# Kernel tuning notes

Measured on AMD Instinct MI355X. Metric: run time of the kernel, lower is better.

Reference implementation:

```python
import jax, jax.numpy as jnp
import numpy as np

B = 64          # number of graph pairs
NODES_PER = 128 # nodes per graph (both sides)
DIM = 256

def setup_inputs() -> dict:
    key = jax.random.key(0)
    k1, k2 = jax.random.split(key)
    N = B * NODES_PER
    left_graph_emb = jax.random.normal(k1, (N, DIM), dtype=jnp.float32)
    right_graph_emb = jax.random.normal(k2, (N, DIM), dtype=jnp.float32)
    # contiguous sorted segment ids, every graph non-empty (matches torch cumsum slicing)
    left_x_batch = jnp.repeat(jnp.arange(B, dtype=jnp.int64), NODES_PER)
    right_x_batch = jnp.repeat(jnp.arange(B, dtype=jnp.int64), NODES_PER)
    return {"left_graph_emb": left_graph_emb, "right_graph_emb": right_graph_emb,
            "left_x_batch": left_x_batch, "right_x_batch": right_x_batch}

def _match(left_emb, right_emb, left_b, right_b):
    # pair mask: node i (left) attends node j (right) only within the same graph
    mask = left_b[:, None] == right_b[None, :]            # [Nl, Nr]
    scores = left_emb @ right_emb.T                        # [Nl, Nr]
    neg = jnp.asarray(-1e30, scores.dtype)
    masked = jnp.where(mask, scores, neg)
    # row softmax (dim=1 in torch) -> right-attended emb per left node
    right_atten = jax.nn.softmax(masked, axis=1) @ right_emb      # [Nl, D]
    # col softmax (dim=0 in torch) -> left-attended emb per right node
    left_atten = jax.nn.softmax(masked, axis=0).T @ left_emb      # [Nr, D]
    # sigmoid gates from inner products
    wl = jax.nn.sigmoid(jnp.sum(left_emb * right_atten, axis=1, keepdims=True))
    wr = jax.nn.sigmoid(jnp.sum(right_emb * left_atten, axis=1, keepdims=True))
    return wl * left_emb, wr * right_emb

def reference(left_graph_emb, right_graph_emb, left_x_batch, right_x_batch):
    ml, mr = _match(left_graph_emb, right_graph_emb, left_x_batch, right_x_batch)
    left_global = jax.ops.segment_sum(ml, left_x_batch, num_segments=B)    # [B, D]
    right_global = jax.ops.segment_sum(mr, right_x_batch, num_segments=B)  # [B, D]
    return left_global, right_global
```

## Files before the change

### kernel.cpp

```cpp
#include <hip/hip_runtime.h>
#include <hip/hip_bf16.h>

#define NGRAPH 64
#define NPER   128
#define DIM    256

typedef __attribute__((ext_vector_type(8))) short bf16x8;
typedef __attribute__((ext_vector_type(4))) float f32x4;

__device__ __forceinline__ float bf2f(short s) {
    union { unsigned u; float f; } v; v.u = ((unsigned)(unsigned short)s) << 16;
    return v.f;
}

__device__ __forceinline__ bf16x8 cvt8(const float4 a, const float4 b) {
    __hip_bfloat162 p0 = __float22bfloat162_rn({a.x, a.y});
    __hip_bfloat162 p1 = __float22bfloat162_rn({a.z, a.w});
    __hip_bfloat162 p2 = __float22bfloat162_rn({b.x, b.y});
    __hip_bfloat162 p3 = __float22bfloat162_rn({b.z, b.w});
    union { __hip_bfloat162 h[4]; bf16x8 v; } u;
    u.h[0] = p0; u.h[1] = p1; u.h[2] = p2; u.h[3] = p3;
    return u.v;
}

__global__ __launch_bounds__(512, 1)
void match_gate_kernel(const float* __restrict__ left,
                       const float* __restrict__ right,
                       float* __restrict__ out) {
    __shared__ __align__(16) short Ls[NPER * DIM];
    __shared__ __align__(16) short Rs[NPER * DIM];
    __shared__ float wq[NPER];
    __shared__ float red[4][128];

    const int j    = blockIdx.x;
    const int g    = (((j >> 5) & 7) << 3) | (j & 7);
    const int sub  = (j >> 3) & 3;
    const int side = sub >> 1;
    const int dh   = sub & 1;

    const float* Lg = left  + (size_t)g * NPER * DIM;
    const float* Rg = right + (size_t)g * NPER * DIM;

    const int tid = threadIdx.x;

    #pragma unroll
    for (int b = 0; b < 4; ++b) {
        const float* src_panel = (b < 2) ? Lg : Rg;
        short* dst_panel = (b < 2) ? Ls : Rs;
        float4 f[8];
        int row[4], k8[4];
        #pragma unroll
        for (int u = 0; u < 4; ++u) {
            const int cc = (b & 1) * 2048 + u * 512 + tid;
            row[u] = cc >> 5;
            k8[u]  = cc & 31;
            const float* s = src_panel + row[u] * DIM + k8[u] * 8;
            f[2 * u]     = *(const float4*)(s);
            f[2 * u + 1] = *(const float4*)(s + 4);
        }
        #pragma unroll
        for (int u = 0; u < 4; ++u) {
            const bf16x8 h = cvt8(f[2 * u], f[2 * u + 1]);
            const int byte = row[u] * (DIM * 2) + ((k8[u] * 16) ^ ((row[u] & 7) << 4));
            *(bf16x8*)((char*)dst_panel + byte) = h;
        }
    }
    __syncthreads();

    const short* Qs = side ? Rs : Ls;
    const short* Ks = side ? Ls : Rs;

    const int wave = tid >> 6;
    const int lane = tid & 63;
    const int row0 = wave * 16;
    const int lr   = lane & 15;
    const int lkb  = (lane >> 4) * 16;

    f32x4 acc[8];
    #pragma unroll
    for (int c = 0; c < 8; ++c) acc[c] = (f32x4){0.f, 0.f, 0.f, 0.f};

    const int arow = row0 + lr;
    const char* aBase = (const char*)Qs + arow * (DIM * 2);
    const int aswz = (arow & 7) << 4;

    #pragma unroll
    for (int ks = 0; ks < 8; ++ks) {
        const bf16x8 a = *(const bf16x8*)(aBase + ((ks * 64 + lkb) ^ aswz));
        #pragma unroll
        for (int c = 0; c < 8; ++c) {
            const int brow = c * 16 + lr;
            const bf16x8 bb = *(const bf16x8*)((const char*)Ks + brow * (DIM * 2)
                                               + ((ks * 64 + lkb) ^ ((brow & 7) << 4)));
            acc[c] = __builtin_amdgcn_mfma_f32_16x16x32_bf16(a, bb, acc[c], 0, 0, 0);
        }
    }

    #pragma unroll
    for (int r = 0; r < 4; ++r) {
        float m = acc[0][r];
        #pragma unroll
        for (int c = 1; c < 8; ++c) m = fmaxf(m, acc[c][r]);
        #pragma unroll
        for (int off = 1; off < 16; off <<= 1) m = fmaxf(m, __shfl_xor(m, off, 64));
        float se = 0.f, wsum = 0.f;
        #pragma unroll
        for (int c = 0; c < 8; ++c) {
            const float e = __expf(acc[c][r] - m);
            se += e; wsum += e * acc[c][r];
        }
        #pragma unroll
        for (int off = 1; off < 16; off <<= 1) {
            se   += __shfl_xor(se, off, 64);
            wsum += __shfl_xor(wsum, off, 64);
        }
        if ((lane & 15) == 0)
            wq[row0 + (lane >> 4) * 4 + r] = 1.f / (1.f + __expf(-(wsum / se)));
    }
    __syncthreads();

    const int dd   = tid & 127;
    const int part = tid >> 7;
    const int dgl  = dh * 128 + dd;
    float sum = 0.f;
    #pragma unroll 8
    for (int i = part * 32; i < part * 32 + 32; ++i) {
        const short s = *(const short*)((const char*)Qs + i * (DIM * 2)
                                        + ((2 * dgl) ^ ((i & 7) << 4)));
        sum += wq[i] * bf2f(s);
    }
    red[part][dd] = sum;
    __syncthreads();
    if (tid < 128) {
        float* outp = out + (size_t)side * (NGRAPH * DIM) + (size_t)g * DIM + dh * 128;
        outp[tid] = red[0][tid] + red[1][tid] + red[2][tid] + red[3][tid];
    }
}

extern "C" void kernel_launch(void* const* d_in, const int* in_sizes, int n_in,
                              void* d_out, int out_size, void* d_ws, size_t ws_size,
                              hipStream_t stream) {
    const float* left  = (const float*)d_in[0];
    const float* right = (const float*)d_in[1];
    float* out = (float*)d_out;
    match_gate_kernel<<<256, 512, 0, stream>>>(left, right, out);
}
```

Measured before the change: 13.21 us.

## Compute row and column softmax gates from one shared score tile per block

Each block now computes the L·R^T score tile once and derives both the row-softmax gates (left side) and the column-softmax gates (right side), merging partial softmax statistics (max, sum, weighted sum) across waves with an online-softmax combine. Blocks grow to 1024 threads split into row tiles and column halves. Each block still recomputes the full GEMM for its graph but writes a 64-wide output quarter for both sides. Before, separate blocks handled the left and right sides, and each one recomputed the GEMM. The change removes that duplicate GEMM work and halves per-thread MFMA accumulators, at the cost of extra shared-memory partial buffers, merge arithmetic and column shuffles.

```diff
diff --git a/kernel.cpp b/kernel.cpp
--- a/kernel.cpp
+++ b/kernel.cpp
@@ -23,20 +23,29 @@
     return u.v;
 }
 
-__global__ __launch_bounds__(512, 1)
-void match_gate_kernel(const float* __restrict__ left,
+__device__ __forceinline__ void sm_merge(float& m, float& se, float& ws,
+                                         float mo, float seo, float wso) {
+    const float M = fmaxf(m, mo);
+    const float a = __expf(m - M), b = __expf(mo - M);
+    se = a * se + b * seo;
+    ws = a * ws + b * wso;
+    m = M;
+}
+
+__global__ __launch_bounds__(1024, 1)
+void match_both_kernel(const float* __restrict__ left,
                        const float* __restrict__ right,
                        float* __restrict__ out) {
     __shared__ __align__(16) short Ls[NPER * DIM];
     __shared__ __align__(16) short Rs[NPER * DIM];
-    __shared__ float wq[NPER];
-    __shared__ float red[4][128];
+    __shared__ float rowpart[2][NPER][3];
+    __shared__ float colpart[8][NPER][3];
+    __shared__ float gl[NPER], gr[NPER];
+    __shared__ float red[2][8][64];
 
-    const int j    = blockIdx.x;
-    const int g    = (((j >> 5) & 7) << 3) | (j & 7);
-    const int sub  = (j >> 3) & 3;
-    const int side = sub >> 1;
-    const int dh   = sub & 1;
+    const int j  = blockIdx.x;
+    const int g  = (((j >> 5) & 7) << 3) | (j & 7);
+    const int dq = (j >> 3) & 3;
 
     const float* Lg = left  + (size_t)g * NPER * DIM;
     const float* Rg = right + (size_t)g * NPER * DIM;
@@ -44,14 +53,14 @@
     const int tid = threadIdx.x;
 
     #pragma unroll
-    for (int b = 0; b < 4; ++b) {
-        const float* src_panel = (b < 2) ? Lg : Rg;
-        short* dst_panel = (b < 2) ? Ls : Rs;
+    for (int b = 0; b < 2; ++b) {
+        const float* src_panel = b ? Rg : Lg;
+        short* dst_panel = b ? Rs : Ls;
         float4 f[8];
         int row[4], k8[4];
         #pragma unroll
         for (int u = 0; u < 4; ++u) {
-            const int cc = (b & 1) * 2048 + u * 512 + tid;
+            const int cc = u * 1024 + tid;
             row[u] = cc >> 5;
             k8[u]  = cc & 31;
             const float* s = src_panel + row[u] * DIM + k8[u] * 8;
@@ -67,45 +76,43 @@
     }
     __syncthreads();
 
-    const short* Qs = side ? Rs : Ls;
-    const short* Ks = side ? Ls : Rs;
-
     const int wave = tid >> 6;
     const int lane = tid & 63;
-    const int row0 = wave * 16;
+    const int t    = wave & 7;
+    const int ch   = wave >> 3;
+    const int row0 = t * 16;
     const int lr   = lane & 15;
     const int lkb  = (lane >> 4) * 16;
 
-    f32x4 acc[8];
+    f32x4 acc[4];
     #pragma unroll
-    for (int c = 0; c < 8; ++c) acc[c] = (f32x4){0.f, 0.f, 0.f, 0.f};
+    for (int c = 0; c < 4; ++c) acc[c] = (f32x4){0.f, 0.f, 0.f, 0.f};
 
     const int arow = row0 + lr;
-    const char* aBase = (const char*)Qs + arow * (DIM * 2);
+    const char* aBase = (const char*)Ls + arow * (DIM * 2);
     const int aswz = (arow & 7) << 4;
 
     #pragma unroll
     for (int ks = 0; ks < 8; ++ks) {
         const bf16x8 a = *(const bf16x8*)(aBase + ((ks * 64 + lkb) ^ aswz));
         #pragma unroll
-        for (int c = 0; c < 8; ++c) {
-            const int brow = c * 16 + lr;
-            const bf16x8 bb = *(const bf16x8*)((const char*)Ks + brow * (DIM * 2)
+        for (int c = 0; c < 4; ++c) {
+            const int brow = ch * 64 + c * 16 + lr;
+            const bf16x8 bb = *(const bf16x8*)((const char*)Rs + brow * (DIM * 2)
                                                + ((ks * 64 + lkb) ^ ((brow & 7) << 4)));
             acc[c] = __builtin_amdgcn_mfma_f32_16x16x32_bf16(a, bb, acc[c], 0, 0, 0);
         }
     }
 
+
     #pragma unroll
     for (int r = 0; r < 4; ++r) {
-        float m = acc[0][r];
-        #pragma unroll
-        for (int c = 1; c < 8; ++c) m = fmaxf(m, acc[c][r]);
+        float m = fmaxf(fmaxf(acc[0][r], acc[1][r]), fmaxf(acc[2][r], acc[3][r]));
         #pragma unroll
         for (int off = 1; off < 16; off <<= 1) m = fmaxf(m, __shfl_xor(m, off, 64));
         float se = 0.f, wsum = 0.f;
         #pragma unroll
-        for (int c = 0; c < 8; ++c) {
+        for (int c = 0; c < 4; ++c) {
             const float e = __expf(acc[c][r] - m);
             se += e; wsum += e * acc[c][r];
         }
@@ -114,26 +121,70 @@
             se   += __shfl_xor(se, off, 64);
             wsum += __shfl_xor(wsum, off, 64);
         }
-        if ((lane & 15) == 0)
-            wq[row0 + (lane >> 4) * 4 + r] = 1.f / (1.f + __expf(-(wsum / se)));
+        if ((lane & 15) == 0) {
+            const int rr = row0 + (lane >> 4) * 4 + r;
+            rowpart[ch][rr][0] = m; rowpart[ch][rr][1] = se; rowpart[ch][rr][2] = wsum;
+        }
+    }
+
+    #pragma unroll
+    for (int c = 0; c < 4; ++c) {
+        float m = fmaxf(fmaxf(acc[c][0], acc[c][1]), fmaxf(acc[c][2], acc[c][3]));
+        float se = 0.f, wsum = 0.f;
+        #pragma unroll
+        for (int r = 0; r < 4; ++r) {
+            const float e = __expf(acc[c][r] - m);
+            se += e; wsum += e * acc[c][r];
+        }
+        #pragma unroll
+        for (int off = 16; off < 64; off <<= 1) {
+            const float mo  = __shfl_xor(m, off, 64);
+            const float seo = __shfl_xor(se, off, 64);
+            const float wso = __shfl_xor(wsum, off, 64);
+            sm_merge(m, se, wsum, mo, seo, wso);
+        }
+        if (lane < 16) {
+            const int jj = ch * 64 + c * 16 + lr;
+            colpart[t][jj][0] = m; colpart[t][jj][1] = se; colpart[t][jj][2] = wsum;
+        }
     }
     __syncthreads();
 
-    const int dd   = tid & 127;
-    const int part = tid >> 7;
-    const int dgl  = dh * 128 + dd;
+    if (tid < NPER) {
+        float m = rowpart[0][tid][0], se = rowpart[0][tid][1], wsum = rowpart[0][tid][2];
+        sm_merge(m, se, wsum, rowpart[1][tid][0], rowpart[1][tid][1], rowpart[1][tid][2]);
+        gl[tid] = 1.f / (1.f + __expf(-(wsum / se)));
+    } else if (tid < 2 * NPER) {
+        const int jj = tid - NPER;
+        float m = colpart[0][jj][0], se = colpart[0][jj][1], wsum = colpart[0][jj][2];
+        #pragma unroll
+        for (int s = 1; s < 8; ++s)
+            sm_merge(m, se, wsum, colpart[s][jj][0], colpart[s][jj][1], colpart[s][jj][2]);
+        gr[jj] = 1.f / (1.f + __expf(-(wsum / se)));
+    }
+    __syncthreads();
+
+    const int side = tid >> 9;
+    const int d    = tid & 63;
+    const int part = (tid >> 6) & 7;
+    const short* P  = side ? Rs : Ls;
+    const float* gg = side ? gr : gl;
+    const int dgl = dq * 64 + d;
     float sum = 0.f;
-    #pragma unroll 8
-    for (int i = part * 32; i < part * 32 + 32; ++i) {
-        const short s = *(const short*)((const char*)Qs + i * (DIM * 2)
+    #pragma unroll
+    for (int i = part * 16; i < part * 16 + 16; ++i) {
+        const short s = *(const short*)((const char*)P + i * (DIM * 2)
                                         + ((2 * dgl) ^ ((i & 7) << 4)));
-        sum += wq[i] * bf2f(s);
+        sum += gg[i] * bf2f(s);
     }
-    red[part][dd] = sum;
+    red[side][part][d] = sum;
     __syncthreads();
     if (tid < 128) {
-        float* outp = out + (size_t)side * (NGRAPH * DIM) + (size_t)g * DIM + dh * 128;
-        outp[tid] = red[0][tid] + red[1][tid] + red[2][tid] + red[3][tid];
+        const int sd = tid >> 6, dd = tid & 63;
+        float s = 0.f;
+        #pragma unroll
+        for (int p = 0; p < 8; ++p) s += red[sd][p][dd];
+        out[(size_t)sd * (NGRAPH * DIM) + (size_t)g * DIM + dq * 64 + dd] = s;
     }
 }
 
@@ -143,5 +194,5 @@
     const float* left  = (const float*)d_in[0];
     const float* right = (const float*)d_in[1];
     float* out = (float*)d_out;
-    match_gate_kernel<<<256, 512, 0, stream>>>(left, right, out);
+    match_both_kernel<<<256, 1024, 0, stream>>>(left, right, out);
 }
```

New measurement: 16.32 us. 23.5% more time.

## Split K-dimension staging to overlap second-half loads with first-half MFMAs

Applied to the files above, without the earlier changes.

The global-to-LDS staging of the L and R panels is split along the feature dimension. The first half of K (columns 0-127) is loaded and converted first, followed by a barrier. The second half is then loaded into registers while the MFMAs for k-steps 0-3 run on the first half, then stored, and after a second barrier the remaining k-steps complete. This hides part of the global load latency behind compute, at the cost of an extra barrier and higher register pressure from holding loads in flight during MFMAs.

```diff
diff --git a/kernel.cpp b/kernel.cpp
--- a/kernel.cpp
+++ b/kernel.cpp
@@ -44,25 +44,24 @@
     const int tid = threadIdx.x;
 
     #pragma unroll
-    for (int b = 0; b < 4; ++b) {
-        const float* src_panel = (b < 2) ? Lg : Rg;
-        short* dst_panel = (b < 2) ? Ls : Rs;
+    for (int b = 0; b < 2; ++b) {
         float4 f[8];
         int row[4], k8[4];
         #pragma unroll
         for (int u = 0; u < 4; ++u) {
-            const int cc = (b & 1) * 2048 + u * 512 + tid;
-            row[u] = cc >> 5;
-            k8[u]  = cc & 31;
-            const float* s = src_panel + row[u] * DIM + k8[u] * 8;
+            const int cc = (b * 4 + u) * 512 + tid;
+            row[u] = (cc >> 4) & 127;
+            k8[u]  = cc & 15;
+            const float* s = (b ? Rg : Lg) + row[u] * DIM + k8[u] * 8;
             f[2 * u]     = *(const float4*)(s);
             f[2 * u + 1] = *(const float4*)(s + 4);
         }
+        short* dst = b ? Rs : Ls;
         #pragma unroll
         for (int u = 0; u < 4; ++u) {
             const bf16x8 h = cvt8(f[2 * u], f[2 * u + 1]);
             const int byte = row[u] * (DIM * 2) + ((k8[u] * 16) ^ ((row[u] & 7) << 4));
-            *(bf16x8*)((char*)dst_panel + byte) = h;
+            *(bf16x8*)((char*)dst + byte) = h;
         }
     }
     __syncthreads();
@@ -84,8 +83,7 @@
     const char* aBase = (const char*)Qs + arow * (DIM * 2);
     const int aswz = (arow & 7) << 4;
 
-    #pragma unroll
-    for (int ks = 0; ks < 8; ++ks) {
+    auto do_mfma = [&](int ks) {
         const bf16x8 a = *(const bf16x8*)(aBase + ((ks * 64 + lkb) ^ aswz));
         #pragma unroll
         for (int c = 0; c < 8; ++c) {
@@ -94,7 +92,49 @@
                                                + ((ks * 64 + lkb) ^ ((brow & 7) << 4)));
             acc[c] = __builtin_amdgcn_mfma_f32_16x16x32_bf16(a, bb, acc[c], 0, 0, 0);
         }
+    };
+
+    {
+        float4 fA[8];
+        int rA[4], kA[4];
+        #pragma unroll
+        for (int u = 0; u < 4; ++u) {
+            const int cc = u * 512 + tid;
+            rA[u] = (cc >> 4) & 127;
+            kA[u] = 16 + (cc & 15);
+            const float* s = Lg + rA[u] * DIM + kA[u] * 8;
+            fA[2 * u]     = *(const float4*)(s);
+            fA[2 * u + 1] = *(const float4*)(s + 4);
+        }
+        do_mfma(0); do_mfma(1);
+        #pragma unroll
+        for (int u = 0; u < 4; ++u) {
+            const bf16x8 h = cvt8(fA[2 * u], fA[2 * u + 1]);
+            const int byte = rA[u] * (DIM * 2) + ((kA[u] * 16) ^ ((rA[u] & 7) << 4));
+            *(bf16x8*)((char*)Ls + byte) = h;
+        }
+        float4 fB[8];
+        int rB[4], kB[4];
+        #pragma unroll
+        for (int u = 0; u < 4; ++u) {
+            const int cc = (4 + u) * 512 + tid;
+            rB[u] = (cc >> 4) & 127;
+            kB[u] = 16 + (cc & 15);
+            const float* s = Rg + rB[u] * DIM + kB[u] * 8;
+            fB[2 * u]     = *(const float4*)(s);
+            fB[2 * u + 1] = *(const float4*)(s + 4);
+        }
+        do_mfma(2); do_mfma(3);
+        #pragma unroll
+        for (int u = 0; u < 4; ++u) {
+            const bf16x8 h = cvt8(fB[2 * u], fB[2 * u + 1]);
+            const int byte = rB[u] * (DIM * 2) + ((kB[u] * 16) ^ ((rB[u] & 7) << 4));
+            *(bf16x8*)((char*)Rs + byte) = h;
+        }
     }
+    __syncthreads();
+
+    do_mfma(4); do_mfma(5); do_mfma(6); do_mfma(7);
 
     #pragma unroll
     for (int r = 0; r < 4; ++r) {
```

After: 12.43 us. 5.9% less time.
